# Kernel tuning notes

Hardware: AMD Instinct MI355X
Metric: run time of the kernel (lower is better)

Reference implementation:

```python
import jax, jax.numpy as jnp
import numpy as np

N, F, H, L = 8192, 256, 16, 8      # nodes, in_dim, hidden_dim, latent_dim
DEPTH = 4
LEAVES = 2 ** DEPTH                # 16 (also the Dense feature width)
C = 10                             # num_classes


def setup_inputs() -> dict:
    key = jax.random.key(0)
    ks = jax.random.split(key, 12)
    X = jax.random.normal(ks[0], (N, F), dtype=jnp.float32)
    # normalized dense adjacency (adj_n); rows roughly sum to ~0.5
    A = jax.random.uniform(ks[1], (N, N), dtype=jnp.float32) / N
    s = 0.05
    W1 = jax.random.normal(ks[2], (F, H), dtype=jnp.float32) * s
    b1 = jnp.zeros((H,), jnp.float32)
    W2 = jax.random.normal(ks[3], (H, L), dtype=jnp.float32) * s
    b2 = jnp.zeros((L,), jnp.float32)
    Wd = jax.random.normal(ks[4], (L, LEAVES), dtype=jnp.float32) * s
    bd = jnp.zeros((LEAVES,), jnp.float32)
    # used_features_mask: permuted identity (used_features_rate == 1.0)
    rng = np.random.default_rng(7)
    perm = rng.permutation(LEAVES)
    mask = jnp.asarray(np.eye(LEAVES, dtype=np.float32)[perm])
    Wdec = jax.random.normal(ks[5], (LEAVES, LEAVES), dtype=jnp.float32) * s
    bdec = jnp.zeros((LEAVES,), jnp.float32)
    pi = jax.random.normal(ks[6], (LEAVES, C), dtype=jnp.float32) * 0.05
    return {"X": X, "A": A, "W1": W1, "b1": b1, "W2": W2, "b2": b2,
            "Wd": Wd, "bd": bd, "mask": mask, "Wdec": Wdec, "bdec": bdec, "pi": pi}


def reference(X, A, W1, b1, W2, b2, Wd, bd, mask, Wdec, bdec, pi):
    # GraphConv: (A @ (X W)) + b, relu  -- spektral applies the dense kernel first
    h = jax.nn.relu(A @ (X @ W1) + b1)            # [N, H]
    z = jax.nn.relu(A @ (h @ W2) + b2)            # [N, L]  (z_mean)
    feat = jax.nn.relu(z @ Wd + bd)               # [N, 16]
    feat = feat @ mask                            # feature permutation
    d = jax.nn.sigmoid(feat @ Wdec + bdec)        # [N, 16] decision probs
    decisions = jnp.stack([d, 1.0 - d], axis=2)   # [N, 16, 2]
    # Faithful to source: mu is re-read from `feat` each level, so only the
    # last level's slice [8:16] actually contributes to the output.
    begin, end = 1, 2
    mu = feat[:, 1:2][:, :, None]
    for level in range(DEPTH):
        mu = feat[:, begin:end][:, :, None]        # [N, 2^level, 1]
        mu = jnp.tile(mu, (1, 1, 2))               # [N, 2^level, 2]
        mu = mu * decisions[:, begin:end, :]
        begin, end = end, end + 2 ** (level + 1)
    mu = mu.reshape(X.shape[0], LEAVES)            # [N, 16]
    probabilities = jax.nn.relu(pi)                # [16, C]
    return mu @ probabilities                      # [N, C]
```

## Files before the change

### kernel.cpp

```cpp
#include <hip/hip_runtime.h>
#include <cstdint>
#include <math.h>

#define BM 16
#define TJ 256

template<int K, int EPI>
__launch_bounds__(256, 2)
__global__ void skinny_gemm(const float* __restrict__ A, int lda, int nj,
                            const float* __restrict__ MT, int ldm,
                            float* __restrict__ out, int ldo,
                            const float* __restrict__ bias,
                            const float* __restrict__ W2)
{
    __shared__ float lds[2][K][TJ];
    const int tid  = threadIdx.x;
    const int lane = tid & 63;
    const int wave = tid >> 6;
    const int row0 = blockIdx.x * BM;

    float acc[4][K];
#pragma unroll
    for (int r = 0; r < 4; ++r)
#pragma unroll
        for (int k = 0; k < K; ++k) acc[r][k] = 0.f;

    const int ntiles = nj / TJ;

#pragma unroll
    for (int i = 0; i < K / 4; ++i) {
        const int k = wave + i * 4;
        const float* g = MT + (size_t)k * ldm + lane * 4;
        __builtin_amdgcn_global_load_lds(
            (const __attribute__((address_space(1))) void*)g,
            (__attribute__((address_space(3))) void*)(&lds[0][k][0]), 16, 0, 0);
    }

    const float* arow[4];
#pragma unroll
    for (int r = 0; r < 4; ++r)
        arow[r] = A + (size_t)(row0 + wave * 4 + r) * lda;

    for (int t = 0; t < ntiles; ++t) {
        __syncthreads();
        const int buf = t & 1;
        if (t + 1 < ntiles) {
#pragma unroll
            for (int i = 0; i < K / 4; ++i) {
                const int k = wave + i * 4;
                const float* g = MT + (size_t)k * ldm + (size_t)(t + 1) * TJ + lane * 4;
                __builtin_amdgcn_global_load_lds(
                    (const __attribute__((address_space(1))) void*)g,
                    (__attribute__((address_space(3))) void*)(&lds[buf ^ 1][k][0]), 16, 0, 0);
            }
        }
        float4 a[4];
#pragma unroll
        for (int r = 0; r < 4; ++r)
            a[r] = *(const float4*)(arow[r] + (size_t)t * TJ + lane * 4);
#pragma unroll
        for (int k = 0; k < K; ++k) {
            const float4 m = *(const float4*)&lds[buf][k][lane * 4];
#pragma unroll
            for (int r = 0; r < 4; ++r)
                acc[r][k] += a[r].x * m.x + a[r].y * m.y + a[r].z * m.z + a[r].w * m.w;
        }
    }

#pragma unroll
    for (int s = 1; s < 64; s <<= 1)
#pragma unroll
        for (int r = 0; r < 4; ++r)
#pragma unroll
            for (int k = 0; k < K; ++k)
                acc[r][k] += __shfl_xor(acc[r][k], s, 64);

    if (EPI == 0) {
        if (lane < K) {
#pragma unroll
            for (int r = 0; r < 4; ++r) {
                float v = acc[r][0];
#pragma unroll
                for (int k = 1; k < K; ++k) if (lane == k) v = acc[r][k];
                out[(size_t)lane * ldo + row0 + wave * 4 + r] = v;
            }
        }
    } else if (EPI == 1) {
        if (lane < 8) {
#pragma unroll
            for (int r = 0; r < 4; ++r) {
                float p = 0.f;
#pragma unroll
                for (int k = 0; k < K; ++k) {
                    float h = acc[r][k] + bias[k];
                    h = h > 0.f ? h : 0.f;
                    p += h * W2[k * 8 + lane];
                }
                out[(size_t)lane * ldo + row0 + wave * 4 + r] = p;
            }
        }
    } else {
        if (lane < 8) {
#pragma unroll
            for (int r = 0; r < 4; ++r) {
                float v = acc[r][0];
#pragma unroll
                for (int k = 1; k < K; ++k) if (lane == k) v = acc[r][k];
                v += bias[lane];
                v = v > 0.f ? v : 0.f;
                out[(size_t)(row0 + wave * 4 + r) * 8 + lane] = v;
            }
        }
    }
}

__global__ void transpose_w1(const float* __restrict__ W1, float* __restrict__ W1T)
{
    const int i = blockIdx.x * 256 + threadIdx.x;
    const int k = i >> 8, c = i & 255;
    W1T[i] = W1[c * 16 + k];
}

__global__ void tree_epilogue(const float* __restrict__ z,
                              const float* __restrict__ Wd,
                              const float* __restrict__ bd,
                              const float* __restrict__ mask,
                              const float* __restrict__ Wdec,
                              const float* __restrict__ bdec,
                              const float* __restrict__ pi,
                              float* __restrict__ out)
{
    const int row = blockIdx.x * blockDim.x + threadIdx.x;
    float zv[8];
#pragma unroll
    for (int k = 0; k < 8; ++k) zv[k] = z[(size_t)row * 8 + k];

    float feat[16];
#pragma unroll
    for (int f = 0; f < 16; ++f) {
        float s = bd[f];
#pragma unroll
        for (int k = 0; k < 8; ++k) s += zv[k] * Wd[k * 16 + f];
        feat[f] = s > 0.f ? s : 0.f;
    }
    float fm[16];
#pragma unroll
    for (int f = 0; f < 16; ++f) {
        float s = 0.f;
#pragma unroll
        for (int g = 0; g < 16; ++g) s += feat[g] * mask[g * 16 + f];
        fm[f] = s;
    }
    float mu[16];
#pragma unroll
    for (int j = 0; j < 8; ++j) {
        const int f = 8 + j;
        float s = bdec[f];
#pragma unroll
        for (int g = 0; g < 16; ++g) s += fm[g] * Wdec[g * 16 + f];
        const float d = 1.f / (1.f + expf(-s));
        mu[2 * j]     = fm[f] * d;
        mu[2 * j + 1] = fm[f] * (1.f - d);
    }
#pragma unroll
    for (int c = 0; c < 10; ++c) {
        float s = 0.f;
#pragma unroll
        for (int m = 0; m < 16; ++m) {
            float p = pi[m * 10 + c];
            p = p > 0.f ? p : 0.f;
            s += mu[m] * p;
        }
        out[(size_t)row * 10 + c] = s;
    }
}

extern "C" void kernel_launch(void* const* d_in, const int* in_sizes, int n_in,
                              void* d_out, int out_size, void* d_ws, size_t ws_size,
                              hipStream_t stream)
{
    const float* X    = (const float*)d_in[0];
    const float* A    = (const float*)d_in[1];
    const float* W1   = (const float*)d_in[2];
    const float* b1   = (const float*)d_in[3];
    const float* W2   = (const float*)d_in[4];
    const float* b2   = (const float*)d_in[5];
    const float* Wd   = (const float*)d_in[6];
    const float* bd   = (const float*)d_in[7];
    const float* mask = (const float*)d_in[8];
    const float* Wdec = (const float*)d_in[9];
    const float* bdec = (const float*)d_in[10];
    const float* pi   = (const float*)d_in[11];
    float* out = (float*)d_out;

    char* ws = (char*)d_ws;
    float* W1T = (float*)ws;
    float* M1T = (float*)(ws + 16 * 1024);
    float* PT  = (float*)(ws + 16 * 1024 + 512 * 1024);
    float* z   = (float*)(ws + 16 * 1024 + 768 * 1024);

    const int N = 8192;

    hipLaunchKernelGGL(transpose_w1, dim3(16), dim3(256), 0, stream, W1, W1T);
    hipLaunchKernelGGL((skinny_gemm<16, 0>), dim3(N / BM), dim3(256), 0, stream,
                       X, 256, 256, W1T, 256, M1T, N, (const float*)nullptr, (const float*)nullptr);
    hipLaunchKernelGGL((skinny_gemm<16, 1>), dim3(N / BM), dim3(256), 0, stream,
                       A, N, N, M1T, N, PT, N, b1, W2);
    hipLaunchKernelGGL((skinny_gemm<8, 2>), dim3(N / BM), dim3(256), 0, stream,
                       A, N, N, PT, N, z, 8, b2, (const float*)nullptr);
    hipLaunchKernelGGL(tree_epilogue, dim3(N / 256), dim3(256), 0, stream,
                       z, Wd, bd, mask, Wdec, bdec, pi, out);
}
```

Measured before the change: 475.9 us.

## Drop LDS staging of skinny operand; register double-buffer A with nontemporal loads

The skinny GEMM stops staging the small transposed matrix in LDS through global_load_lds and no longer calls __syncthreads per tile. Each wave now reads that matrix straight from global memory and relies on L2/L1 caching. The big A rows are double-buffered in registers with nontemporal loads, so the streaming adjacency reads avoid polluting the cache and the next tile's loads overlap with compute. The cost is more global and cache traffic for the shared operand, since each wave reloads it, and more registers for the second A buffer.

```diff
diff --git a/kernel.cpp b/kernel.cpp
--- a/kernel.cpp
+++ b/kernel.cpp
@@ -2,8 +2,7 @@
 #include <cstdint>
 #include <math.h>
 
-#define BM 16
-#define TJ 256
+typedef float f32x4 __attribute__((ext_vector_type(4)));
 
 template<int K, int EPI>
 __launch_bounds__(256, 2)
@@ -13,11 +12,9 @@
                             const float* __restrict__ bias,
                             const float* __restrict__ W2)
 {
-    __shared__ float lds[2][K][TJ];
-    const int tid  = threadIdx.x;
-    const int lane = tid & 63;
-    const int wave = tid >> 6;
-    const int row0 = blockIdx.x * BM;
+    const int lane = (int)(threadIdx.x & 63);
+    const int wave = (int)(threadIdx.x >> 6);
+    const int row0 = blockIdx.x * 16 + wave * 4;
 
     float acc[4][K];
 #pragma unroll
@@ -25,45 +22,56 @@
 #pragma unroll
         for (int k = 0; k < K; ++k) acc[r][k] = 0.f;
 
-    const int ntiles = nj / TJ;
-
-#pragma unroll
-    for (int i = 0; i < K / 4; ++i) {
-        const int k = wave + i * 4;
-        const float* g = MT + (size_t)k * ldm + lane * 4;
-        __builtin_amdgcn_global_load_lds(
-            (const __attribute__((address_space(1))) void*)g,
-            (__attribute__((address_space(3))) void*)(&lds[0][k][0]), 16, 0, 0);
-    }
-
-    const float* arow[4];
+    const int ntiles = nj / 256;
+
+    const float* ap[4];
 #pragma unroll
     for (int r = 0; r < 4; ++r)
-        arow[r] = A + (size_t)(row0 + wave * 4 + r) * lda;
-
-    for (int t = 0; t < ntiles; ++t) {
-        __syncthreads();
-        const int buf = t & 1;
+        ap[r] = A + (size_t)(row0 + r) * lda + lane * 4;
+    const float* mp = MT + lane * 4;
+
+    f32x4 a0[4], a1[4];
+#pragma unroll
+    for (int r = 0; r < 4; ++r)
+        a0[r] = __builtin_nontemporal_load((const f32x4*)(ap[r]));
+    if (ntiles > 1) {
+#pragma unroll
+        for (int r = 0; r < 4; ++r)
+            a1[r] = __builtin_nontemporal_load((const f32x4*)(ap[r] + 256));
+    }
+
+    for (int t = 0; t < ntiles; t += 2) {
+        {
+            const float* mt = mp + (size_t)t * 256;
+#pragma unroll
+            for (int k = 0; k < K; ++k) {
+                const f32x4 m = *(const f32x4*)(mt + (size_t)k * ldm);
+#pragma unroll
+                for (int r = 0; r < 4; ++r)
+                    acc[r][k] += a0[r].x * m.x + a0[r].y * m.y
+                               + a0[r].z * m.z + a0[r].w * m.w;
+            }
+            if (t + 2 < ntiles) {
+#pragma unroll
+                for (int r = 0; r < 4; ++r)
+                    a0[r] = __builtin_nontemporal_load((const f32x4*)(ap[r] + (size_t)(t + 2) * 256));
+            }
+        }
         if (t + 1 < ntiles) {
-#pragma unroll
-            for (int i = 0; i < K / 4; ++i) {
-                const int k = wave + i * 4;
-                const float* g = MT + (size_t)k * ldm + (size_t)(t + 1) * TJ + lane * 4;
-                __builtin_amdgcn_global_load_lds(
-                    (const __attribute__((address_space(1))) void*)g,
-                    (__attribute__((address_space(3))) void*)(&lds[buf ^ 1][k][0]), 16, 0, 0);
-            }
-        }
-        float4 a[4];
-#pragma unroll
-        for (int r = 0; r < 4; ++r)
-            a[r] = *(const float4*)(arow[r] + (size_t)t * TJ + lane * 4);
-#pragma unroll
-        for (int k = 0; k < K; ++k) {
-            const float4 m = *(const float4*)&lds[buf][k][lane * 4];
-#pragma unroll
-            for (int r = 0; r < 4; ++r)
-                acc[r][k] += a[r].x * m.x + a[r].y * m.y + a[r].z * m.z + a[r].w * m.w;
+            const float* mt = mp + (size_t)(t + 1) * 256;
+#pragma unroll
+            for (int k = 0; k < K; ++k) {
+                const f32x4 m = *(const f32x4*)(mt + (size_t)k * ldm);
+#pragma unroll
+                for (int r = 0; r < 4; ++r)
+                    acc[r][k] += a1[r].x * m.x + a1[r].y * m.y
+                               + a1[r].z * m.z + a1[r].w * m.w;
+            }
+            if (t + 3 < ntiles) {
+#pragma unroll
+                for (int r = 0; r < 4; ++r)
+                    a1[r] = __builtin_nontemporal_load((const f32x4*)(ap[r] + (size_t)(t + 3) * 256));
+            }
         }
     }
 
@@ -82,7 +90,7 @@
                 float v = acc[r][0];
 #pragma unroll
                 for (int k = 1; k < K; ++k) if (lane == k) v = acc[r][k];
-                out[(size_t)lane * ldo + row0 + wave * 4 + r] = v;
+                out[(size_t)lane * ldo + row0 + r] = v;
             }
         }
     } else if (EPI == 1) {
@@ -96,7 +104,7 @@
                     h = h > 0.f ? h : 0.f;
                     p += h * W2[k * 8 + lane];
                 }
-                out[(size_t)lane * ldo + row0 + wave * 4 + r] = p;
+                out[(size_t)lane * ldo + row0 + r] = p;
             }
         }
     } else {
@@ -108,7 +116,7 @@
                 for (int k = 1; k < K; ++k) if (lane == k) v = acc[r][k];
                 v += bias[lane];
                 v = v > 0.f ? v : 0.f;
-                out[(size_t)(row0 + wave * 4 + r) * 8 + lane] = v;
+                out[(size_t)(row0 + r) * 8 + lane] = v;
             }
         }
     }
@@ -202,11 +210,11 @@
     const int N = 8192;
 
     hipLaunchKernelGGL(transpose_w1, dim3(16), dim3(256), 0, stream, W1, W1T);
-    hipLaunchKernelGGL((skinny_gemm<16, 0>), dim3(N / BM), dim3(256), 0, stream,
+    hipLaunchKernelGGL((skinny_gemm<16, 0>), dim3(N / 16), dim3(256), 0, stream,
                        X, 256, 256, W1T, 256, M1T, N, (const float*)nullptr, (const float*)nullptr);
-    hipLaunchKernelGGL((skinny_gemm<16, 1>), dim3(N / BM), dim3(256), 0, stream,
+    hipLaunchKernelGGL((skinny_gemm<16, 1>), dim3(N / 16), dim3(256), 0, stream,
                        A, N, N, M1T, N, PT, N, b1, W2);
-    hipLaunchKernelGGL((skinny_gemm<8, 2>), dim3(N / BM), dim3(256), 0, stream,
+    hipLaunchKernelGGL((skinny_gemm<8, 2>), dim3(N / 16), dim3(256), 0, stream,
                        A, N, N, PT, N, z, 8, b2, (const float*)nullptr);
     hipLaunchKernelGGL(tree_epilogue, dim3(N / 256), dim3(256), 0, stream,
                        z, Wd, bd, mask, Wdec, bdec, pi, out);
```

Result: no change. 481.8 us (+1.2%).

## Split the A-GEMMs along the reduction axis and reduce partial sums in epilogue kernels

Applied to the files above, without the earlier changes.

The two A-streaming skinny GEMMs now tile the reduction dimension into 8 chunks of 1024 columns (grid N/16 x 8). Each block stages its whole M slice into LDS once, and the A loads become nontemporal and double-buffered in registers. Partial sums go to workspace and are combined by new reduce kernels that also apply bias, ReLU and the W2 projection or the tree epilogue. This raises block-level parallelism and removes the per-tile barrier loop over the long reduction. The cost is extra partial-sum traffic and one more kernel launch.

```diff
diff --git a/kernel.cpp b/kernel.cpp
--- a/kernel.cpp
+++ b/kernel.cpp
@@ -2,65 +2,72 @@
 #include <cstdint>
 #include <math.h>
 
-#define BM 16
-#define TJ 256
-
-template<int K, int EPI>
+typedef float f32x4 __attribute__((ext_vector_type(4)));
+
+template<int K, int JB, int EPI>
 __launch_bounds__(256, 2)
-__global__ void skinny_gemm(const float* __restrict__ A, int lda, int nj,
+__global__ void skinny_gemm(const float* __restrict__ A, int lda,
                             const float* __restrict__ MT, int ldm,
-                            float* __restrict__ out, int ldo,
-                            const float* __restrict__ bias,
-                            const float* __restrict__ W2)
-{
-    __shared__ float lds[2][K][TJ];
-    const int tid  = threadIdx.x;
+                            float* __restrict__ out, int N)
+{
+    __shared__ float lds[K * JB];
+    const int tid  = (int)threadIdx.x;
     const int lane = tid & 63;
     const int wave = tid >> 6;
-    const int row0 = blockIdx.x * BM;
-
-    float acc[4][K];
-#pragma unroll
-    for (int r = 0; r < 4; ++r)
-#pragma unroll
-        for (int k = 0; k < K; ++k) acc[r][k] = 0.f;
-
-    const int ntiles = nj / TJ;
-
-#pragma unroll
-    for (int i = 0; i < K / 4; ++i) {
-        const int k = wave + i * 4;
-        const float* g = MT + (size_t)k * ldm + lane * 4;
+    const int row0 = blockIdx.x * 16 + wave * 4;
+    const int j0   = blockIdx.y * JB;
+
+    constexpr int STAGE_ITERS = (K * JB) / (256 * 4);
+#pragma unroll
+    for (int i = 0; i < STAGE_ITERS; ++i) {
+        const int fbase = i * 1024 + wave * 256;
+        const int k  = fbase / JB;
+        const int jj = fbase % JB;
+        const float* g = MT + (size_t)k * ldm + j0 + jj + lane * 4;
         __builtin_amdgcn_global_load_lds(
             (const __attribute__((address_space(1))) void*)g,
-            (__attribute__((address_space(3))) void*)(&lds[0][k][0]), 16, 0, 0);
-    }
-
-    const float* arow[4];
+            (__attribute__((address_space(3))) void*)(lds + fbase),
+            16, 0, 0);
+    }
+    __syncthreads();
+
+    float acc[4][K];
 #pragma unroll
     for (int r = 0; r < 4; ++r)
-        arow[r] = A + (size_t)(row0 + wave * 4 + r) * lda;
-
-    for (int t = 0; t < ntiles; ++t) {
-        __syncthreads();
-        const int buf = t & 1;
-        if (t + 1 < ntiles) {
-#pragma unroll
-            for (int i = 0; i < K / 4; ++i) {
-                const int k = wave + i * 4;
-                const float* g = MT + (size_t)k * ldm + (size_t)(t + 1) * TJ + lane * 4;
-                __builtin_amdgcn_global_load_lds(
-                    (const __attribute__((address_space(1))) void*)g,
-                    (__attribute__((address_space(3))) void*)(&lds[buf ^ 1][k][0]), 16, 0, 0);
-            }
-        }
-        float4 a[4];
+#pragma unroll
+        for (int k = 0; k < K; ++k) acc[r][k] = 0.f;
+
+    const float* ap[4];
+#pragma unroll
+    for (int r = 0; r < 4; ++r)
+        ap[r] = A + (size_t)(row0 + r) * lda + j0 + lane * 4;
+
+    constexpr int JS = JB / 256;
+    f32x4 abuf[2][4];
+#pragma unroll
+    for (int r = 0; r < 4; ++r)
+        abuf[0][r] = __builtin_nontemporal_load((const f32x4*)(ap[r]));
+    if (JS > 1) {
 #pragma unroll
         for (int r = 0; r < 4; ++r)
-            a[r] = *(const float4*)(arow[r] + (size_t)t * TJ + lane * 4);
+            abuf[1][r] = __builtin_nontemporal_load((const f32x4*)(ap[r] + 256));
+    }
+
+#pragma unroll
+    for (int js = 0; js < JS; ++js) {
+        const int cur = js & 1;
+        f32x4 a[4];
+#pragma unroll
+        for (int r = 0; r < 4; ++r) a[r] = abuf[cur][r];
+        if (js + 2 < JS) {
+#pragma unroll
+            for (int r = 0; r < 4; ++r)
+                abuf[cur][r] = __builtin_nontemporal_load((const f32x4*)(ap[r] + (size_t)(js + 2) * 256));
+        }
+        const float* mrow = lds + js * 256 + lane * 4;
 #pragma unroll
         for (int k = 0; k < K; ++k) {
-            const float4 m = *(const float4*)&lds[buf][k][lane * 4];
+            const f32x4 m = *(const f32x4*)(mrow + k * JB);
 #pragma unroll
             for (int r = 0; r < 4; ++r)
                 acc[r][k] += a[r].x * m.x + a[r].y * m.y + a[r].z * m.z + a[r].w * m.w;
@@ -75,41 +82,16 @@
             for (int k = 0; k < K; ++k)
                 acc[r][k] += __shfl_xor(acc[r][k], s, 64);
 
-    if (EPI == 0) {
-        if (lane < K) {
-#pragma unroll
-            for (int r = 0; r < 4; ++r) {
-                float v = acc[r][0];
-#pragma unroll
-                for (int k = 1; k < K; ++k) if (lane == k) v = acc[r][k];
-                out[(size_t)lane * ldo + row0 + wave * 4 + r] = v;
-            }
-        }
-    } else if (EPI == 1) {
-        if (lane < 8) {
-#pragma unroll
-            for (int r = 0; r < 4; ++r) {
-                float p = 0.f;
-#pragma unroll
-                for (int k = 0; k < K; ++k) {
-                    float h = acc[r][k] + bias[k];
-                    h = h > 0.f ? h : 0.f;
-                    p += h * W2[k * 8 + lane];
-                }
-                out[(size_t)lane * ldo + row0 + wave * 4 + r] = p;
-            }
-        }
-    } else {
-        if (lane < 8) {
-#pragma unroll
-            for (int r = 0; r < 4; ++r) {
-                float v = acc[r][0];
-#pragma unroll
-                for (int k = 1; k < K; ++k) if (lane == k) v = acc[r][k];
-                v += bias[lane];
-                v = v > 0.f ? v : 0.f;
-                out[(size_t)(row0 + wave * 4 + r) * 8 + lane] = v;
-            }
+    if (lane < K) {
+#pragma unroll
+        for (int r = 0; r < 4; ++r) {
+            float v = acc[r][0];
+#pragma unroll
+            for (int k = 1; k < K; ++k) if (lane == k) v = acc[r][k];
+            if (EPI == 0)
+                out[(size_t)lane * N + row0 + r] = v;
+            else
+                out[((size_t)blockIdx.y * K + lane) * N + row0 + r] = v;
         }
     }
 }
@@ -121,20 +103,50 @@
     W1T[i] = W1[c * 16 + k];
 }
 
-__global__ void tree_epilogue(const float* __restrict__ z,
-                              const float* __restrict__ Wd,
-                              const float* __restrict__ bd,
-                              const float* __restrict__ mask,
-                              const float* __restrict__ Wdec,
-                              const float* __restrict__ bdec,
-                              const float* __restrict__ pi,
-                              float* __restrict__ out)
-{
-    const int row = blockIdx.x * blockDim.x + threadIdx.x;
+__global__ void reduce_epi1(const float* __restrict__ part1,
+                            const float* __restrict__ b1,
+                            const float* __restrict__ W2,
+                            float* __restrict__ PT, int N)
+{
+    const int row = blockIdx.x * 256 + threadIdx.x;
+    float h[16];
+#pragma unroll
+    for (int k = 0; k < 16; ++k) {
+        float s = b1[k];
+#pragma unroll
+        for (int jb = 0; jb < 8; ++jb)
+            s += part1[((size_t)jb * 16 + k) * N + row];
+        h[k] = s > 0.f ? s : 0.f;
+    }
+#pragma unroll
+    for (int k2 = 0; k2 < 8; ++k2) {
+        float p = 0.f;
+#pragma unroll
+        for (int k = 0; k < 16; ++k) p += h[k] * W2[k * 8 + k2];
+        PT[(size_t)k2 * N + row] = p;
+    }
+}
+
+__global__ void reduce_epi2_tree(const float* __restrict__ part2,
+                                 const float* __restrict__ b2,
+                                 const float* __restrict__ Wd,
+                                 const float* __restrict__ bd,
+                                 const float* __restrict__ mask,
+                                 const float* __restrict__ Wdec,
+                                 const float* __restrict__ bdec,
+                                 const float* __restrict__ pi,
+                                 float* __restrict__ out, int N)
+{
+    const int row = blockIdx.x * 256 + threadIdx.x;
     float zv[8];
 #pragma unroll
-    for (int k = 0; k < 8; ++k) zv[k] = z[(size_t)row * 8 + k];
-
+    for (int k = 0; k < 8; ++k) {
+        float s = b2[k];
+#pragma unroll
+        for (int jb = 0; jb < 8; ++jb)
+            s += part2[((size_t)jb * 8 + k) * N + row];
+        zv[k] = s > 0.f ? s : 0.f;
+    }
     float feat[16];
 #pragma unroll
     for (int f = 0; f < 16; ++f) {
@@ -193,21 +205,22 @@
     const float* pi   = (const float*)d_in[11];
     float* out = (float*)d_out;
 
+    const int N = 8192;
     char* ws = (char*)d_ws;
-    float* W1T = (float*)ws;
-    float* M1T = (float*)(ws + 16 * 1024);
-    float* PT  = (float*)(ws + 16 * 1024 + 512 * 1024);
-    float* z   = (float*)(ws + 16 * 1024 + 768 * 1024);
-
-    const int N = 8192;
+    float* W1T   = (float*)ws;                             ws += 16 * 1024;
+    float* M1T   = (float*)ws;                             ws += 512 * 1024;
+    float* PT    = (float*)ws;                             ws += 256 * 1024;
+    float* part1 = (float*)ws;                             ws += 8 * 16 * N * 4;
+    float* part2 = (float*)ws;
 
     hipLaunchKernelGGL(transpose_w1, dim3(16), dim3(256), 0, stream, W1, W1T);
-    hipLaunchKernelGGL((skinny_gemm<16, 0>), dim3(N / BM), dim3(256), 0, stream,
-                       X, 256, 256, W1T, 256, M1T, N, (const float*)nullptr, (const float*)nullptr);
-    hipLaunchKernelGGL((skinny_gemm<16, 1>), dim3(N / BM), dim3(256), 0, stream,
-                       A, N, N, M1T, N, PT, N, b1, W2);
-    hipLaunchKernelGGL((skinny_gemm<8, 2>), dim3(N / BM), dim3(256), 0, stream,
-                       A, N, N, PT, N, z, 8, b2, (const float*)nullptr);
-    hipLaunchKernelGGL(tree_epilogue, dim3(N / 256), dim3(256), 0, stream,
-                       z, Wd, bd, mask, Wdec, bdec, pi, out);
-}
+    hipLaunchKernelGGL((skinny_gemm<16, 256, 0>), dim3(N / 16, 1), dim3(256), 0, stream,
+                       X, 256, W1T, 256, M1T, N);
+    hipLaunchKernelGGL((skinny_gemm<16, 1024, 3>), dim3(N / 16, 8), dim3(256), 0, stream,
+                       A, N, M1T, N, part1, N);
+    hipLaunchKernelGGL(reduce_epi1, dim3(N / 256), dim3(256), 0, stream, part1, b1, W2, PT, N);
+    hipLaunchKernelGGL((skinny_gemm<8, 1024, 3>), dim3(N / 16, 8), dim3(256), 0, stream,
+                       A, N, PT, N, part2, N);
+    hipLaunchKernelGGL(reduce_epi2_tree, dim3(N / 256), dim3(256), 0, stream,
+                       part2, b2, Wd, bd, mask, Wdec, bdec, pi, out, N);
+}
```

New measurement: 600.3 us. 1.26x slower.
